# Optimization experiments

Hardware: AMD Instinct MI355X
Metric: run time of the kernel (lower is better)

## Reference

```python
import jax, jax.numpy as jnp
import numpy as np

B_, S_, IN_, D_, N_, K_ = 16, 4096, 64, 256, 16, 32


def _ln(x, g, b):
    m = jnp.mean(x, axis=-1, keepdims=True)
    v = jnp.var(x, axis=-1, keepdims=True)
    return (x - m) * jax.lax.rsqrt(v + 1e-5) * g + b


def setup_inputs() -> dict:
    key = jax.random.key(0)
    ks = jax.random.split(key, 24)
    s = 0.02
    d = dict(
        x=jax.random.normal(ks[0], (B_, S_, IN_), jnp.float32),
        W_in=jax.random.normal(ks[1], (IN_, D_)) * s, b_in=jnp.zeros((D_,)),
        ln1_g=jnp.ones((D_,)), ln1_b=jnp.zeros((D_,)),
        conv_w=jax.random.normal(ks[2], (D_, 1, 3)) * s, conv_b=jnp.zeros((D_,)),
        Wd=jax.random.normal(ks[3], (D_, D_)) * s, bd=jnp.zeros((D_,)),
        WB=jax.random.normal(ks[4], (D_, N_)) * s, bB=jnp.zeros((N_,)),
        WC=jax.random.normal(ks[5], (D_, N_)) * s, bC=jnp.zeros((N_,)),
        A=-jax.random.uniform(ks[6], (D_, N_)),
        Wg=jax.random.normal(ks[7], (D_, D_)) * s, bg=jnp.zeros((D_,)),
        filt_re=jax.random.normal(ks[8], (K_, D_)) * s,
        filt_im=jax.random.normal(ks[9], (K_, D_)) * s,
        alpha=jnp.ones((D_,)), beta=jnp.ones((D_,)),
        lnc_g=jnp.ones((D_,)), lnc_b=jnp.zeros((D_,)),
        W1=jax.random.normal(ks[10], (D_, D_ // 2)) * s, b1=jnp.zeros((D_ // 2,)),
        W2=jax.random.normal(ks[11], (D_ // 2, 2)) * s, b2=jnp.zeros((2,)),
    )
    return d


def reference(x, W_in, b_in, ln1_g, ln1_b, conv_w, conv_b, Wd, bd, WB, bB, WC, bC,
              A, Wg, bg, filt_re, filt_im, alpha, beta, lnc_g, lnc_b, W1, b1, W2, b2):
    xp = x @ W_in + b_in                                   # [B,S,D]

    # ---- TemporalBlock ----
    xn = _ln(xp, ln1_g, ln1_b)
    xc = jax.lax.conv_general_dilated(
        jnp.swapaxes(xn, 1, 2), conv_w, (1,), [(1, 1)],
        feature_group_count=D_, dimension_numbers=('NCH', 'OIH', 'NCH'))
    xc = jnp.swapaxes(xc + conv_b[:, None], 1, 2)          # [B,S,D]
    u = jax.nn.silu(xc)

    delta = jax.nn.softplus(u @ Wd + bd)                   # [B,S,D]
    Bm = u @ WB + bB                                       # [B,S,N]
    Cm = u @ WC + bC                                       # [B,S,N]

    def step(h, inp):
        u_t, d_t, B_t, C_t = inp                           # [B,D],[B,D],[B,N],[B,N]
        h = (1.0 + d_t[:, :, None] * A) * h + d_t[:, :, None] * B_t[:, None, :] * u_t[:, :, None]
        y_t = jnp.sum(C_t[:, None, :] * h, axis=-1)        # [B,D]
        return h, y_t

    h0 = jnp.zeros((u.shape[0], D_, N_), u.dtype)
    xs = tuple(jnp.swapaxes(a, 0, 1) for a in (u, delta, Bm, Cm))
    _, ys = jax.lax.scan(step, h0, xs)
    x_ssm = jnp.swapaxes(ys, 0, 1)                         # [B,S,D]
    g = jax.nn.silu(xn @ Wg + bg)
    x_t = xp + x_ssm * g

    # ---- SpectralBlock ----
    Xf = jnp.fft.rfft(xp, axis=1)                          # [B,F,D] complex
    mag = jnp.abs(Xf)
    _, idx = jax.lax.top_k(jnp.swapaxes(mag, 1, 2), K_)    # [B,D,K]
    idx = jnp.swapaxes(idx, 1, 2)                          # [B,K,D]
    sel = jnp.take_along_axis(Xf, idx, axis=1)             # [B,K,D]
    filt = filt_re + 1j * filt_im                          # [K,D]
    filtered = sel * filt[None]
    bi = jnp.arange(Xf.shape[0])[:, None, None]
    di = jnp.arange(D_)[None, None, :]
    Xfil = jnp.zeros_like(Xf).at[bi, idx, di].set(filtered)
    x_f = jnp.fft.irfft(Xfil, n=xp.shape[1], axis=1)       # [B,S,D]

    # ---- Fusion + classifier (eval: dropout = identity) ----
    z = alpha * x_t + beta * x_f
    zp = jnp.mean(z, axis=1)                               # [B,D]
    hcls = jax.nn.relu(_ln(zp, lnc_g, lnc_b) @ W1 + b1)
    return hcls @ W2 + b2                                  # [B,2]
```

## Files before the change

kernel.cpp:

```cpp
#include <hip/hip_runtime.h>
#include <hip/hip_bf16.h>
#include <math.h>

#define BB 16
#define SS 4096
#define IN 64
#define DD 256
#define NN 16
#define KK 32
#define CH 64
#define LCH 64
#define BS (BB*SS)

typedef __attribute__((ext_vector_type(4))) float f32x4;
typedef __attribute__((ext_vector_type(8))) short bf16x8;

__device__ __forceinline__ float bf2f(unsigned short u){
  return __uint_as_float(((unsigned int)u)<<16);
}
__device__ __forceinline__ unsigned short f2bf(float f){
  unsigned int u = __float_as_uint(f);
  return (unsigned short)((u + 0x7fffu + ((u>>16)&1u)) >> 16);
}
__device__ __forceinline__ float fast_softplus(float v){
  float e = __expf(-fabsf(v));
  return fmaxf(v, 0.f) + __logf(1.f + e);
}
__device__ __forceinline__ float fast_silu(float v){
  return v * __builtin_amdgcn_rcpf(1.f + __expf(-v));
}
__device__ __forceinline__ void* swz(void* base, int row, int byteoff){
  return (void*)((char*)base + (row<<9) + (byteoff ^ ((row&7)<<4)));
}
#define SW(i) ((i) ^ (((i)>>4)&15))
__device__ __forceinline__ int rev4(int k){
  return ((k&3)<<10) | (((k>>2)&3)<<8) | (((k>>4)&3)<<6)
       | (((k>>6)&3)<<4) | (((k>>8)&3)<<2) | ((k>>10)&3);
}

__global__ void k_prep(const float* Wd, const float* Wg, const float* WB, const float* WC,
                       const float* W_in, const float* bBv, const float* bCv,
                       unsigned short* WdF, unsigned short* WgF, unsigned short* WinF,
                       float* bbc, float2* tw){
  int id = blockIdx.x*256 + threadIdx.x;
  if (id < 73728){
    int jn = id >> 12; int rem = id & 4095;
    int kc = rem >> 9; int l8 = (rem >> 3) & 63; int e = id & 7;
    int lr = l8 & 15, lh = l8 >> 4;
    int k = kc*32 + lh*8 + e;
    float v;
    if (jn < 16){ int n = jn*16 + lr; v = Wd[k*256+n]; }
    else { int c = (jn-16)*16 + lr; v = (c<16) ? WB[k*16+c] : WC[k*16+(c-16)]; }
    WdF[id] = f2bf(v);
  }
  else if (id < 139264){
    int o = id - 73728;
    int jn = o >> 12; int rem = o & 4095;
    int kc = rem >> 9; int l8 = (rem >> 3) & 63; int e = o & 7;
    int lr = l8 & 15, lh = l8 >> 4;
    int k = kc*32 + lh*8 + e;
    WgF[o] = f2bf(Wg[k*256 + jn*16 + lr]);
  }
  else if (id < 155648){
    int o = id - 139264;
    int jn = o >> 10; int rem = o & 1023;
    int kc = rem >> 9; int l8 = (rem >> 3) & 63; int e = o & 7;
    int lr = l8 & 15, lh = l8 >> 4;
    int k = kc*32 + lh*8 + e;
    WinF[o] = f2bf(W_in[k*256 + jn*16 + lr]);
  }
  else if (id < 157696){ int k = id-155648;
    double a = -6.283185307179586476925287 * (double)k / 4096.0;
    tw[k] = make_float2((float)cos(a), (float)sin(a)); }
  else if (id < 157728){ int j = id-157696; bbc[j] = (j<16)? bBv[j] : bCv[j-16]; }
}

__global__ __launch_bounds__(256) void k_front(const float* x, const unsigned short* WinF, const float* b_in,
      const float* ln1_g, const float* ln1_b, const float* conv_w, const float* conv_b,
      float2* xpz, unsigned short* xn16, unsigned short* u16){
  __shared__ unsigned short xb[32*64];
  __shared__ float xs[20][260];
  int tid = threadIdx.x;
  int b = blockIdx.y; int t0 = blockIdx.x*16;
  {
    int row = tid>>3, slot = tid&7;
    int t = t0 - 1 + row;
    unsigned short h[8];
    if (row < 18 && t >= 0 && t < SS){
      const float* src = &x[((size_t)b*SS + t)*IN + slot*8];
      float4 v0 = *(const float4*)src;
      float4 v1 = *(const float4*)(src+4);
      h[0]=f2bf(v0.x); h[1]=f2bf(v0.y); h[2]=f2bf(v0.z); h[3]=f2bf(v0.w);
      h[4]=f2bf(v1.x); h[5]=f2bf(v1.y); h[6]=f2bf(v1.z); h[7]=f2bf(v1.w);
    } else {
      #pragma unroll
      for (int i=0;i<8;i++) h[i]=0;
    }
    *(uint4*)&xb[row*64 + ((slot ^ (row&7))<<3)] = *(uint4*)h;
  }
  __syncthreads();
  int wv = tid>>6, lane = tid&63, lr = lane&15, lh = lane>>4;
  {
    bf16x8 af[2][2];
    #pragma unroll
    for (int rf=0;rf<2;rf++)
      #pragma unroll
      for (int kc=0;kc<2;kc++){
        int row = rf*16 + lr;
        int slot = (kc*4 + lh) ^ (row&7);
        af[rf][kc] = *(const bf16x8*)&xb[row*64 + slot*8];
      }
    f32x4 acc[2][4];
    #pragma unroll
    for (int rf=0;rf<2;rf++)
      #pragma unroll
      for (int jj=0;jj<4;jj++){ acc[rf][jj][0]=0.f; acc[rf][jj][1]=0.f; acc[rf][jj][2]=0.f; acc[rf][jj][3]=0.f; }
    #pragma unroll
    for (int jj=0;jj<4;jj++){
      int jn = wv*4 + jj;
      const bf16x8* bp = (const bf16x8*)(WinF + (size_t)jn*1024 + (size_t)lane*8);
      bf16x8 b0 = bp[0];
      bf16x8 b1 = bp[64];
      #pragma unroll
      for (int rf=0;rf<2;rf++){
        acc[rf][jj] = __builtin_amdgcn_mfma_f32_16x16x32_bf16(af[rf][0], b0, acc[rf][jj], 0,0,0);
        acc[rf][jj] = __builtin_amdgcn_mfma_f32_16x16x32_bf16(af[rf][1], b1, acc[rf][jj], 0,0,0);
      }
    }
    #pragma unroll
    for (int jj=0;jj<4;jj++){
      int col = (wv*4+jj)*16 + lr;
      float bs = b_in[col];
      #pragma unroll
      for (int rf=0;rf<2;rf++){
        #pragma unroll
        for (int i=0;i<4;i++){
          int row = rf*16 + lh*4 + i;
          if (row < 18) xs[row][col] = acc[rf][jj][i] + bs;
        }
      }
    }
  }
  __syncthreads();
  {
    int sl = tid&15, p0 = tid>>4;
    float2* dst = xpz + (size_t)b*128*SS + t0 + sl;
    #pragma unroll
    for (int pass=0; pass<8; pass++){
      int p = p0 + 16*pass;
      float2 v = *(const float2*)&xs[1+sl][2*p];
      dst[(size_t)p*SS] = v;
    }
  }
  __syncthreads();
  float4 lg4 = *(const float4*)&ln1_g[lane*4];
  float4 lb4 = *(const float4*)&ln1_b[lane*4];
  for (int r=wv; r<18; r+=4){
    int t = t0 - 1 + r;
    bool valid = (t>=0) && (t<SS);
    float4 v = *(const float4*)&xs[r][lane*4];
    float s1 = v.x+v.y+v.z+v.w;
    float s2 = v.x*v.x+v.y*v.y+v.z*v.z+v.w*v.w;
    #pragma unroll
    for (int off=32; off; off>>=1){ s1 += __shfl_xor(s1,off); s2 += __shfl_xor(s2,off); }
    float mean = s1*(1.f/256.f);
    float var  = s2*(1.f/256.f) - mean*mean;
    float rstd = rsqrtf(var + 1e-5f);
    float o0 = valid ? ((v.x-mean)*rstd*lg4.x + lb4.x) : 0.f;
    float o1 = valid ? ((v.y-mean)*rstd*lg4.y + lb4.y) : 0.f;
    float o2 = valid ? ((v.z-mean)*rstd*lg4.z + lb4.z) : 0.f;
    float o3 = valid ? ((v.w-mean)*rstd*lg4.w + lb4.w) : 0.f;
    *(float4*)&xs[r][lane*4] = make_float4(o0,o1,o2,o3);
    if (r>=1 && r<=16){
      ushort4 st;
      st.x=f2bf(o0); st.y=f2bf(o1); st.z=f2bf(o2); st.w=f2bf(o3);
      *(ushort4*)&xn16[((size_t)b*SS + t)*DD + lane*4] = st;
    }
  }
  __syncthreads();
  int d = tid;
  float w0=conv_w[d*3], w1=conv_w[d*3+1], w2=conv_w[d*3+2], cb=conv_b[d];
  #pragma unroll 4
  for (int rr=0; rr<16; rr++){
    float a0=xs[rr][d], a1=xs[rr+1][d], a2=xs[rr+2][d];
    float xc = a0*w0 + a1*w1 + a2*w2 + cb;
    u16[((size_t)b*SS + (t0+rr))*DD + d] = f2bf(fast_silu(xc));
  }
}

template<int NTOT, int ACT>
__global__ __launch_bounds__(512,2) void k_gemm2(const unsigned short* Ab, const unsigned short* Bt,
      const float* bias_main, const float* bias_bc,
      unsigned short* out_main, unsigned short* out_bc){
  __shared__ unsigned short As[64*256];
  const int NF = NTOT/2;
  int tid = threadIdx.x;
  int m0 = blockIdx.x*64;
  {
    const uint4* gA = (const uint4*)(Ab + (size_t)m0*256);
    #pragma unroll
    for (int i=0;i<4;i++){
      int f = tid + 512*i;
      uint4 v = gA[f];
      *(uint4*)swz(As, f>>5, (f&31)<<4) = v;
    }
  }
  __syncthreads();
  int wv = tid>>6, lane = tid&63;
  int wm = wv>>1, nh = wv&1;
  int lr = lane&15, lh = lane>>4;
  const bf16x8* bbase = (const bf16x8*)(Bt + (size_t)(nh*NF)*4096 + (size_t)lane*8);
  f32x4 acc[NF];
  #pragma unroll
  for (int j=0;j<NF;j++){ acc[j][0]=0.f; acc[j][1]=0.f; acc[j][2]=0.f; acc[j][3]=0.f; }
  bf16x8 bq[2][8];
  #pragma unroll
  for (int kc=0;kc<8;kc++) bq[0][kc] = bbase[kc*64];
  #pragma unroll
  for (int j=0;j<NF;j++){
    if (j+1 < NF){
      #pragma unroll
      for (int kc=0;kc<8;kc++) bq[(j+1)&1][kc] = bbase[(j+1)*512 + kc*64];
    }
    #pragma unroll
    for (int kc=0;kc<8;kc++){
      bf16x8 af = *(const bf16x8*)swz(As, wm*16+lr, kc*64+lh*16);
      acc[j] = __builtin_amdgcn_mfma_f32_16x16x32_bf16(af, bq[j&1][kc], acc[j], 0,0,0);
    }
  }
  #pragma unroll
  for (int j=0;j<NF;j++){
    int jn = nh*NF + j;
    if (jn < 16){
      int col = jn*16 + lr;
      float bs = bias_main[col];
      #pragma unroll
      for (int i=0;i<4;i++){
        int row = m0 + wm*16 + lh*4 + i;
        float v = acc[j][i] + bs;
        if (ACT==1) v = fast_softplus(v);
        if (ACT==2) v = fast_silu(v);
        out_main[(size_t)row*256 + col] = f2bf(v);
      }
    } else {
      int col = (jn-16)*16 + lr;
      float bs = bias_bc[col];
      #pragma unroll
      for (int i=0;i<4;i++){
        int row = m0 + wm*16 + lh*4 + i;
        out_bc[(size_t)row*32 + col] = f2bf(acc[j][i] + bs);
      }
    }
  }
}

__global__ __launch_bounds__(256,4) void k_fft(const float2* xpz, const float2* twg, int* rank, float* T0){
  __shared__ float2 buf[4096];
  __shared__ int scr8[8];
  int blk = blockIdx.x;
  int b = blk >> 7, pair = blk & 127;
  int tid = threadIdx.x;
  const float4* src4 = (const float4*)(xpz + ((size_t)b*128 + pair)*SS);
  #pragma unroll
  for (int q=tid; q<2048; q+=256){
    float4 v = src4[q];
    buf[SW(2*q)]   = make_float2(v.x, v.y);
    buf[SW(2*q+1)] = make_float2(v.z, v.w);
  }
  __syncthreads();
  int m = 1024, fac = 1;
  for (int st=0; st<6; st++){
    #pragma unroll
    for (int it=0; it<4; it++){
      int t = tid + 256*it;
      int j = t & (m-1);
      int i0 = 4*t - 3*j;
      float2 a0 = buf[SW(i0)];
      float2 a1 = buf[SW(i0+m)];
      float2 a2 = buf[SW(i0+2*m)];
      float2 a3 = buf[SW(i0+3*m)];
      float2 w1 = twg[j*fac];
      float2 w2 = make_float2(fmaf(w1.x,w1.x,-w1.y*w1.y), 2.f*w1.x*w1.y);
      float2 w3 = make_float2(fmaf(w1.x,w2.x,-w1.y*w2.y), fmaf(w1.x,w2.y, w1.y*w2.x));
      float t0x=a0.x+a2.x, t0y=a0.y+a2.y;
      float t1x=a0.x-a2.x, t1y=a0.y-a2.y;
      float t2x=a1.x+a3.x, t2y=a1.y+a3.y;
      float t3x=a1.y-a3.y, t3y=a3.x-a1.x;
      buf[SW(i0)]     = make_float2(t0x+t2x, t0y+t2y);
      float b1x = t1x+t3x, b1y = t1y+t3y;
      buf[SW(i0+m)]   = make_float2(fmaf(w1.x,b1x,-w1.y*b1y), fmaf(w1.x,b1y, w1.y*b1x));
      float b2x = t0x-t2x, b2y = t0y-t2y;
      buf[SW(i0+2*m)] = make_float2(fmaf(w2.x,b2x,-w2.y*b2y), fmaf(w2.x,b2y, w2.y*b2x));
      float b3x = t1x-t3x, b3y = t1y-t3y;
      buf[SW(i0+3*m)] = make_float2(fmaf(w3.x,b3x,-w3.y*b3y), fmaf(w3.x,b3y, w3.y*b3x));
    }
    __syncthreads();
    m >>= 2; fac <<= 2;
  }
  float2 z0 = buf[0];
  float thx = 4.f*z0.x*z0.x, thy = 4.f*z0.y*z0.y;
  int cx=0, cy=0;
  #pragma unroll
  for (int j=0;j<8;j++){
    int f = 1 + tid + 256*j;
    float2 zf = buf[SW(rev4(f))];
    float2 zc = buf[SW(rev4(4096-f))];
    float sxr = zf.x+zc.x, sxi = zf.y-zc.y;
    float syr = zf.x-zc.x, syi = zf.y+zc.y;
    cx += (fmaf(sxr,sxr,sxi*sxi) > thx) ? 1 : 0;
    cy += (fmaf(syr,syr,syi*syi) > thy) ? 1 : 0;
  }
  #pragma unroll
  for (int off=32; off; off>>=1){ cx += __shfl_xor(cx, off); cy += __shfl_xor(cy, off); }
  if ((tid&63)==0){ scr8[tid>>6] = cx; scr8[4+(tid>>6)] = cy; }
  __syncthreads();
  if (tid==0){
    int r0 = b*256 + 2*pair;
    rank[r0]   = scr8[0]+scr8[1]+scr8[2]+scr8[3];
    rank[r0+1] = scr8[4]+scr8[5]+scr8[6]+scr8[7];
    T0[r0]   = z0.x;
    T0[r0+1] = z0.y;
  }
}

__global__ __launch_bounds__(512) void k_scanA(const unsigned short* d16, const unsigned short* u16,
      const unsigned short* bc16, const float* Aw, float* AB_A, float* AB_B){
  __shared__ float bcs[LCH][16];
  int c = blockIdx.x, b = blockIdx.y;
  int t0 = c*LCH;
  int tid = threadIdx.x;
  {
    int t = tid>>3, q = tid&7;
    unsigned int v = *(const unsigned int*)(bc16 + ((size_t)b*SS + t0 + t)*32 + q*2);
    bcs[t][q*2]   = bf2f((unsigned short)(v & 0xffff));
    bcs[t][q*2+1] = bf2f((unsigned short)(v >> 16));
  }
  __syncthreads();
  int d = tid & 255, hf = tid >> 8;
  float aw[8];
  #pragma unroll
  for (int j=0;j<2;j++){
    float4 a4 = *(const float4*)&Aw[d*16 + hf*8 + j*4];
    aw[4*j]=a4.x; aw[4*j+1]=a4.y; aw[4*j+2]=a4.z; aw[4*j+3]=a4.w;
  }
  float Ac[8], Bc[8];
  #pragma unroll
  for (int n=0;n<8;n++){ Ac[n]=1.f; Bc[n]=0.f; }
  const unsigned short* dp = d16 + ((size_t)b*SS + t0)*DD + d;
  const unsigned short* up = u16 + ((size_t)b*SS + t0)*DD + d;
  #pragma unroll 8
  for (int t=0;t<LCH;t++){
    float de = bf2f(dp[(size_t)t*DD]);
    float uu = bf2f(up[(size_t)t*DD]);
    float du = de*uu;
    float4 b0 = *(const float4*)&bcs[t][hf*8];
    float4 b1 = *(const float4*)&bcs[t][hf*8+4];
    float bm[8] = {b0.x,b0.y,b0.z,b0.w, b1.x,b1.y,b1.z,b1.w};
    #pragma unroll
    for (int n=0;n<8;n++){
      float a = fmaf(de, aw[n], 1.f);
      Ac[n] *= a;
      Bc[n] = fmaf(a, Bc[n], du*bm[n]);
    }
  }
  size_t o = (size_t)c*65536 + (size_t)b*4096 + (size_t)d*16 + hf*8;
  #pragma unroll
  for (int j=0;j<2;j++){
    *(float4*)&AB_A[o+4*j] = make_float4(Ac[4*j],Ac[4*j+1],Ac[4*j+2],Ac[4*j+3]);
    *(float4*)&AB_B[o+4*j] = make_float4(Bc[4*j],Bc[4*j+1],Bc[4*j+2],Bc[4*j+3]);
  }
}

__global__ void k_scanB(const float* AB_A, const float* AB_B, float* Hs){
  int tid = blockIdx.x*256 + threadIdx.x;
  float h = 0.f;
  #pragma unroll 8
  for (int c=0;c<CH;c++){
    Hs[c*65536 + tid] = h;
    h = fmaf(AB_A[c*65536 + tid], h, AB_B[c*65536 + tid]);
  }
}

__global__ __launch_bounds__(512) void k_scanC(const unsigned short* d16, const unsigned short* u16,
      const unsigned short* bc16, const unsigned short* g16, const float* Aw, const float* Hs, float* part){
  __shared__ float bcs[LCH][32];
  __shared__ float scr[256];
  int c = blockIdx.x, b = blockIdx.y;
  int t0 = c*LCH;
  int tid = threadIdx.x;
  {
    int t = tid>>3, q = tid&7;
    uint2 v = *(const uint2*)(bc16 + ((size_t)b*SS + t0 + t)*32 + q*4);
    bcs[t][q*4]   = bf2f((unsigned short)(v.x & 0xffff));
    bcs[t][q*4+1] = bf2f((unsigned short)(v.x >> 16));
    bcs[t][q*4+2] = bf2f((unsigned short)(v.y & 0xffff));
    bcs[t][q*4+3] = bf2f((unsigned short)(v.y >> 16));
  }
  __syncthreads();
  int d = tid & 255, hf = tid >> 8;
  float aw[8];
  #pragma unroll
  for (int j=0;j<2;j++){
    float4 a4 = *(const float4*)&Aw[d*16 + hf*8 + j*4];
    aw[4*j]=a4.x; aw[4*j+1]=a4.y; aw[4*j+2]=a4.z; aw[4*j+3]=a4.w;
  }
  float h[8];
  {
    size_t o = (size_t)c*65536 + (size_t)b*4096 + (size_t)d*16 + hf*8;
    #pragma unroll
    for (int j=0;j<2;j++){
      float4 h4 = *(const float4*)&Hs[o+4*j];
      h[4*j]=h4.x; h[4*j+1]=h4.y; h[4*j+2]=h4.z; h[4*j+3]=h4.w;
    }
  }
  float acc = 0.f;
  const unsigned short* dp = d16 + ((size_t)b*SS + t0)*DD + d;
  const unsigned short* up = u16 + ((size_t)b*SS + t0)*DD + d;
  const unsigned short* gp = g16 + ((size_t)b*SS + t0)*DD + d;
  #pragma unroll 8
  for (int t=0;t<LCH;t++){
    float de = bf2f(dp[(size_t)t*DD]);
    float uu = bf2f(up[(size_t)t*DD]);
    float gg = bf2f(gp[(size_t)t*DD]);
    float du = de*uu;
    float4 b0 = *(const float4*)&bcs[t][hf*8];
    float4 b1 = *(const float4*)&bcs[t][hf*8+4];
    float4 c0 = *(const float4*)&bcs[t][16+hf*8];
    float4 c1 = *(const float4*)&bcs[t][16+hf*8+4];
    float bm[8] = {b0.x,b0.y,b0.z,b0.w, b1.x,b1.y,b1.z,b1.w};
    float cm[8] = {c0.x,c0.y,c0.z,c0.w, c1.x,c1.y,c1.z,c1.w};
    float y0 = 0.f, y1 = 0.f;
    #pragma unroll
    for (int n=0;n<8;n+=2){
      float a0 = fmaf(de, aw[n],   1.f);
      float a1 = fmaf(de, aw[n+1], 1.f);
      h[n]   = fmaf(a0, h[n],   du*bm[n]);
      h[n+1] = fmaf(a1, h[n+1], du*bm[n+1]);
      y0 = fmaf(cm[n],   h[n],   y0);
      y1 = fmaf(cm[n+1], h[n+1], y1);
    }
    acc = fmaf(y0+y1, gg, acc);
  }
  if (hf==1) scr[d] = acc;
  __syncthreads();
  if (hf==0) part[(size_t)(b*256 + d)*CH + c] = acc + scr[d];
}

__global__ __launch_bounds__(256) void k_final(const float* part, const float* T0, const int* rank,
      const float* alpha, const float* beta, const float* filt_re,
      const float* lnc_g, const float* lnc_b,
      const float* W1, const float* b1, const float* W2, const float* b2,
      float* out){
  __shared__ float zs[256];
  __shared__ float h1[128];
  __shared__ float red[8];
  int b = blockIdx.x, d = threadIdx.x;
  int row = b*256 + d;
  float ps = 0.f;
  #pragma unroll 8
  for (int c=0;c<CH;c++) ps += part[(size_t)row*CH + c];
  float ssm_mean = ps * (1.f/4096.f);
  float t0v = T0[row];
  float mxp = t0v * (1.f/4096.f);
  int r = rank[row];
  float spec = (r < KK) ? t0v * filt_re[r*DD + d] * (1.f/4096.f) : 0.f;
  float zp = alpha[d]*(mxp + ssm_mean) + beta[d]*spec;
  float s1 = zp, s2 = zp*zp;
  #pragma unroll
  for (int off=32; off; off>>=1){ s1 += __shfl_xor(s1,off); s2 += __shfl_xor(s2,off); }
  if ((d&63)==0){ red[d>>6] = s1; red[4+(d>>6)] = s2; }
  __syncthreads();
  float mean = (red[0]+red[1]+red[2]+red[3]) * (1.f/256.f);
  float var  = (red[4]+red[5]+red[6]+red[7]) * (1.f/256.f) - mean*mean;
  float ln = (zp-mean)*rsqrtf(var+1e-5f)*lnc_g[d] + lnc_b[d];
  zs[d] = ln;
  __syncthreads();
  if (d < 128){
    float acc = b1[d];
    #pragma unroll 16
    for (int k=0;k<256;k++) acc = fmaf(zs[k], W1[k*128+d], acc);
    h1[d] = fmaxf(acc, 0.f);
  }
  __syncthreads();
  if (d < 2){
    float acc = b2[d];
    #pragma unroll 16
    for (int k=0;k<128;k++) acc = fmaf(h1[k], W2[k*2+d], acc);
    out[b*2+d] = acc;
  }
}

extern "C" void kernel_launch(void* const* d_in, const int* in_sizes, int n_in,
                              void* d_out, int out_size, void* d_ws, size_t ws_size,
                              hipStream_t stream){
  const float* x      = (const float*)d_in[0];
  const float* W_in   = (const float*)d_in[1];
  const float* b_in   = (const float*)d_in[2];
  const float* ln1_g  = (const float*)d_in[3];
  const float* ln1_b  = (const float*)d_in[4];
  const float* conv_w = (const float*)d_in[5];
  const float* conv_b = (const float*)d_in[6];
  const float* Wd     = (const float*)d_in[7];
  const float* bd     = (const float*)d_in[8];
  const float* WB     = (const float*)d_in[9];
  const float* bB     = (const float*)d_in[10];
  const float* WC     = (const float*)d_in[11];
  const float* bC     = (const float*)d_in[12];
  const float* A      = (const float*)d_in[13];
  const float* Wg     = (const float*)d_in[14];
  const float* bg     = (const float*)d_in[15];
  const float* filt_re= (const float*)d_in[16];
  const float* alpha  = (const float*)d_in[18];
  const float* beta   = (const float*)d_in[19];
  const float* lnc_g  = (const float*)d_in[20];
  const float* lnc_b  = (const float*)d_in[21];
  const float* W1     = (const float*)d_in[22];
  const float* b1     = (const float*)d_in[23];
  const float* W2     = (const float*)d_in[24];
  const float* b2     = (const float*)d_in[25];

  char* w = (char*)d_ws;
  unsigned short* d16  = (unsigned short*)(w);
  unsigned short* bc16 = (unsigned short*)(w + 33554432);
  float2* xpz = (float2*)(w + 67108864);
  float* AB_A = (float*)(w + 67108864);
  float* AB_B = (float*)(w + 67108864 + 16777216);
  float* Hs   = (float*)(w + 67108864 + 33554432);
  float* part = (float*)(w + 67108864 + 50331648);
  unsigned short* xn16 = (unsigned short*)(w + 134217728);
  unsigned short* u16  = (unsigned short*)(w + 167772160);
  unsigned short* g16  = (unsigned short*)(w + 201326592);
  char* small = w + 234881024;
  unsigned short* WdF  = (unsigned short*)(small);
  unsigned short* WgF  = (unsigned short*)(small + 147456);
  unsigned short* WinF = (unsigned short*)(small + 278528);
  float*  bbc = (float*)(small + 311296);
  float2* tw  = (float2*)(small + 311424);
  float*  T0  = (float*)(small + 327808);
  int*    rank= (int*)(small + 344192);
  (void)in_sizes; (void)n_in; (void)out_size; (void)ws_size;

  hipLaunchKernelGGL(k_prep, dim3(617), dim3(256), 0, stream,
                     Wd, Wg, WB, WC, W_in, bB, bC, WdF, WgF, WinF, bbc, tw);
  hipLaunchKernelGGL(k_front, dim3(SS/16, BB), dim3(256), 0, stream,
                     x, WinF, b_in, ln1_g, ln1_b, conv_w, conv_b, xpz, xn16, u16);
  hipLaunchKernelGGL(k_fft, dim3(BB*128), dim3(256), 0, stream, xpz, tw, rank, T0);
  hipLaunchKernelGGL((k_gemm2<18,1>), dim3(BS/64), dim3(512), 0, stream,
                     u16, WdF, bd, bbc, d16, bc16);
  hipLaunchKernelGGL((k_gemm2<16,2>), dim3(BS/64), dim3(512), 0, stream,
                     xn16, WgF, bg, bbc, g16, bc16);
  hipLaunchKernelGGL(k_scanA, dim3(CH, BB), dim3(512), 0, stream, d16, u16, bc16, A, AB_A, AB_B);
  hipLaunchKernelGGL(k_scanB, dim3(256), dim3(256), 0, stream, AB_A, AB_B, Hs);
  hipLaunchKernelGGL(k_scanC, dim3(CH, BB), dim3(512), 0, stream, d16, u16, bc16, g16, A, Hs, part);
  hipLaunchKernelGGL(k_final, dim3(BB), dim3(256), 0, stream,
                     part, T0, rank, alpha, beta, filt_re, lnc_g, lnc_b, W1, b1, W2, b2, (float*)d_out);
}
```

Measured before the change: 251.8 us.

## Store delta, delta*u and gate transposed time-major for vectorized scan loads

The GEMM epilogues now write delta, delta*u (using u already staged in shared memory) and the silu gate in a [B,D,S] transposed layout with 4-wide stores. The scan kernels then read 8 consecutive timesteps per 16-byte load per channel, instead of strided scalar bf16 loads across D, and no longer reload u. The bc16 buffer is moved to make room. In exchange the GEMM stores are strided across channels and less coalesced, and du is rounded to bf16 after the multiply.

```diff
diff --git a/kernel.cpp b/kernel.cpp
--- a/kernel.cpp
+++ b/kernel.cpp
@@ -191,7 +191,7 @@
 template<int NTOT, int ACT>
 __global__ __launch_bounds__(512,2) void k_gemm2(const unsigned short* Ab, const unsigned short* Bt,
       const float* bias_main, const float* bias_bc,
-      unsigned short* out_main, unsigned short* out_bc){
+      unsigned short* outT, unsigned short* duT, unsigned short* out_bc){
   __shared__ unsigned short As[64*256];
   const int NF = NTOT/2;
   int tid = threadIdx.x;
@@ -228,19 +228,33 @@
       acc[j] = __builtin_amdgcn_mfma_f32_16x16x32_bf16(af, bq[j&1][kc], acc[j], 0,0,0);
     }
   }
+  int row0 = m0 + wm*16 + lh*4;
+  int bb = row0 >> 12, tb = row0 & 4095;
   #pragma unroll
   for (int j=0;j<NF;j++){
     int jn = nh*NF + j;
     if (jn < 16){
       int col = jn*16 + lr;
       float bs = bias_main[col];
-      #pragma unroll
-      for (int i=0;i<4;i++){
-        int row = m0 + wm*16 + lh*4 + i;
-        float v = acc[j][i] + bs;
-        if (ACT==1) v = fast_softplus(v);
-        if (ACT==2) v = fast_silu(v);
-        out_main[(size_t)row*256 + col] = f2bf(v);
+      if (ACT==1){
+        ushort4 de4, du4;
+        unsigned short* dep = (unsigned short*)&de4;
+        unsigned short* dup = (unsigned short*)&du4;
+        #pragma unroll
+        for (int i=0;i<4;i++){
+          float de = fast_softplus(acc[j][i] + bs);
+          float uu = bf2f(*(const unsigned short*)swz(As, wm*16+lh*4+i, col*2));
+          dep[i] = f2bf(de);
+          dup[i] = f2bf(de*uu);
+        }
+        *(ushort4*)&outT[((size_t)bb*256 + col)*SS + tb] = de4;
+        *(ushort4*)&duT [((size_t)bb*256 + col)*SS + tb] = du4;
+      } else {
+        ushort4 g4;
+        unsigned short* gp = (unsigned short*)&g4;
+        #pragma unroll
+        for (int i=0;i<4;i++) gp[i] = f2bf(fast_silu(acc[j][i] + bs));
+        *(ushort4*)&outT[((size_t)bb*256 + col)*SS + tb] = g4;
       }
     } else {
       int col = (jn-16)*16 + lr;
@@ -323,7 +337,7 @@
   }
 }
 
-__global__ __launch_bounds__(512) void k_scanA(const unsigned short* d16, const unsigned short* u16,
+__global__ __launch_bounds__(512) void k_scanA(const unsigned short* deT, const unsigned short* duT,
       const unsigned short* bc16, const float* Aw, float* AB_A, float* AB_B){
   __shared__ float bcs[LCH][16];
   int c = blockIdx.x, b = blockIdx.y;
@@ -346,21 +360,41 @@
   float Ac[8], Bc[8];
   #pragma unroll
   for (int n=0;n<8;n++){ Ac[n]=1.f; Bc[n]=0.f; }
-  const unsigned short* dp = d16 + ((size_t)b*SS + t0)*DD + d;
-  const unsigned short* up = u16 + ((size_t)b*SS + t0)*DD + d;
-  #pragma unroll 8
-  for (int t=0;t<LCH;t++){
-    float de = bf2f(dp[(size_t)t*DD]);
-    float uu = bf2f(up[(size_t)t*DD]);
-    float du = de*uu;
-    float4 b0 = *(const float4*)&bcs[t][hf*8];
-    float4 b1 = *(const float4*)&bcs[t][hf*8+4];
-    float bm[8] = {b0.x,b0.y,b0.z,b0.w, b1.x,b1.y,b1.z,b1.w};
-    #pragma unroll
-    for (int n=0;n<8;n++){
-      float a = fmaf(de, aw[n], 1.f);
-      Ac[n] *= a;
-      Bc[n] = fmaf(a, Bc[n], du*bm[n]);
+  const uint4* dp4 = (const uint4*)(deT + ((size_t)(b*256+d))*SS + t0);
+  const uint4* up4 = (const uint4*)(duT + ((size_t)(b*256+d))*SS + t0);
+  uint4 dv[2], uv[2];
+  dv[0] = dp4[0]; uv[0] = up4[0];
+  #pragma unroll
+  for (int q8=0; q8<8; q8++){
+    int cur = q8&1;
+    if (q8 < 7){ dv[cur^1] = dp4[q8+1]; uv[cur^1] = up4[q8+1]; }
+    const unsigned int* dw = (const unsigned int*)&dv[cur];
+    const unsigned int* uw = (const unsigned int*)&uv[cur];
+    #pragma unroll
+    for (int e=0;e<4;e++){
+      int t = q8*8 + e*2;
+      float de0 = __uint_as_float(dw[e]<<16);
+      float de1 = __uint_as_float(dw[e]&0xffff0000u);
+      float du0 = __uint_as_float(uw[e]<<16);
+      float du1 = __uint_as_float(uw[e]&0xffff0000u);
+      float4 b0 = *(const float4*)&bcs[t][hf*8];
+      float4 b1 = *(const float4*)&bcs[t][hf*8+4];
+      float4 b2 = *(const float4*)&bcs[t+1][hf*8];
+      float4 b3 = *(const float4*)&bcs[t+1][hf*8+4];
+      float bm0[8] = {b0.x,b0.y,b0.z,b0.w, b1.x,b1.y,b1.z,b1.w};
+      float bm1[8] = {b2.x,b2.y,b2.z,b2.w, b3.x,b3.y,b3.z,b3.w};
+      #pragma unroll
+      for (int n=0;n<8;n++){
+        float a = fmaf(de0, aw[n], 1.f);
+        Ac[n] *= a;
+        Bc[n] = fmaf(a, Bc[n], du0*bm0[n]);
+      }
+      #pragma unroll
+      for (int n=0;n<8;n++){
+        float a = fmaf(de1, aw[n], 1.f);
+        Ac[n] *= a;
+        Bc[n] = fmaf(a, Bc[n], du1*bm1[n]);
+      }
     }
   }
   size_t o = (size_t)c*65536 + (size_t)b*4096 + (size_t)d*16 + hf*8;
@@ -381,8 +415,8 @@
   }
 }
 
-__global__ __launch_bounds__(512) void k_scanC(const unsigned short* d16, const unsigned short* u16,
-      const unsigned short* bc16, const unsigned short* g16, const float* Aw, const float* Hs, float* part){
+__global__ __launch_bounds__(512) void k_scanC(const unsigned short* deT, const unsigned short* duT,
+      const unsigned short* bc16, const unsigned short* gT, const float* Aw, const float* Hs, float* part){
   __shared__ float bcs[LCH][32];
   __shared__ float scr[256];
   int c = blockIdx.x, b = blockIdx.y;
@@ -414,32 +448,66 @@
     }
   }
   float acc = 0.f;
-  const unsigned short* dp = d16 + ((size_t)b*SS + t0)*DD + d;
-  const unsigned short* up = u16 + ((size_t)b*SS + t0)*DD + d;
-  const unsigned short* gp = g16 + ((size_t)b*SS + t0)*DD + d;
-  #pragma unroll 8
-  for (int t=0;t<LCH;t++){
-    float de = bf2f(dp[(size_t)t*DD]);
-    float uu = bf2f(up[(size_t)t*DD]);
-    float gg = bf2f(gp[(size_t)t*DD]);
-    float du = de*uu;
-    float4 b0 = *(const float4*)&bcs[t][hf*8];
-    float4 b1 = *(const float4*)&bcs[t][hf*8+4];
-    float4 c0 = *(const float4*)&bcs[t][16+hf*8];
-    float4 c1 = *(const float4*)&bcs[t][16+hf*8+4];
-    float bm[8] = {b0.x,b0.y,b0.z,b0.w, b1.x,b1.y,b1.z,b1.w};
-    float cm[8] = {c0.x,c0.y,c0.z,c0.w, c1.x,c1.y,c1.z,c1.w};
-    float y0 = 0.f, y1 = 0.f;
-    #pragma unroll
-    for (int n=0;n<8;n+=2){
-      float a0 = fmaf(de, aw[n],   1.f);
-      float a1 = fmaf(de, aw[n+1], 1.f);
-      h[n]   = fmaf(a0, h[n],   du*bm[n]);
-      h[n+1] = fmaf(a1, h[n+1], du*bm[n+1]);
-      y0 = fmaf(cm[n],   h[n],   y0);
-      y1 = fmaf(cm[n+1], h[n+1], y1);
-    }
-    acc = fmaf(y0+y1, gg, acc);
+  const uint4* dp4 = (const uint4*)(deT + ((size_t)(b*256+d))*SS + t0);
+  const uint4* up4 = (const uint4*)(duT + ((size_t)(b*256+d))*SS + t0);
+  const uint4* gp4 = (const uint4*)(gT  + ((size_t)(b*256+d))*SS + t0);
+  uint4 dv[2], uv[2], gv[2];
+  dv[0] = dp4[0]; uv[0] = up4[0]; gv[0] = gp4[0];
+  #pragma unroll
+  for (int q8=0; q8<8; q8++){
+    int cur = q8&1;
+    if (q8 < 7){ dv[cur^1] = dp4[q8+1]; uv[cur^1] = up4[q8+1]; gv[cur^1] = gp4[q8+1]; }
+    const unsigned int* dw = (const unsigned int*)&dv[cur];
+    const unsigned int* uw = (const unsigned int*)&uv[cur];
+    const unsigned int* gw = (const unsigned int*)&gv[cur];
+    #pragma unroll
+    for (int e=0;e<4;e++){
+      int t = q8*8 + e*2;
+      float de0 = __uint_as_float(dw[e]<<16);
+      float de1 = __uint_as_float(dw[e]&0xffff0000u);
+      float du0 = __uint_as_float(uw[e]<<16);
+      float du1 = __uint_as_float(uw[e]&0xffff0000u);
+      float gg0 = __uint_as_float(gw[e]<<16);
+      float gg1 = __uint_as_float(gw[e]&0xffff0000u);
+      {
+        float4 b0 = *(const float4*)&bcs[t][hf*8];
+        float4 b1 = *(const float4*)&bcs[t][hf*8+4];
+        float4 c0 = *(const float4*)&bcs[t][16+hf*8];
+        float4 c1 = *(const float4*)&bcs[t][16+hf*8+4];
+        float bm[8] = {b0.x,b0.y,b0.z,b0.w, b1.x,b1.y,b1.z,b1.w};
+        float cm[8] = {c0.x,c0.y,c0.z,c0.w, c1.x,c1.y,c1.z,c1.w};
+        float y0 = 0.f, y1 = 0.f;
+        #pragma unroll
+        for (int n=0;n<8;n+=2){
+          float a0 = fmaf(de0, aw[n],   1.f);
+          float a1 = fmaf(de0, aw[n+1], 1.f);
+          h[n]   = fmaf(a0, h[n],   du0*bm[n]);
+          h[n+1] = fmaf(a1, h[n+1], du0*bm[n+1]);
+          y0 = fmaf(cm[n],   h[n],   y0);
+          y1 = fmaf(cm[n+1], h[n+1], y1);
+        }
+        acc = fmaf(y0+y1, gg0, acc);
+      }
+      {
+        float4 b0 = *(const float4*)&bcs[t+1][hf*8];
+        float4 b1 = *(const float4*)&bcs[t+1][hf*8+4];
+        float4 c0 = *(const float4*)&bcs[t+1][16+hf*8];
+        float4 c1 = *(const float4*)&bcs[t+1][16+hf*8+4];
+        float bm[8] = {b0.x,b0.y,b0.z,b0.w, b1.x,b1.y,b1.z,b1.w};
+        float cm[8] = {c0.x,c0.y,c0.z,c0.w, c1.x,c1.y,c1.z,c1.w};
+        float y0 = 0.f, y1 = 0.f;
+        #pragma unroll
+        for (int n=0;n<8;n+=2){
+          float a0 = fmaf(de1, aw[n],   1.f);
+          float a1 = fmaf(de1, aw[n+1], 1.f);
+          h[n]   = fmaf(a0, h[n],   du1*bm[n]);
+          h[n+1] = fmaf(a1, h[n+1], du1*bm[n+1]);
+          y0 = fmaf(cm[n],   h[n],   y0);
+          y1 = fmaf(cm[n+1], h[n+1], y1);
+        }
+        acc = fmaf(y0+y1, gg1, acc);
+      }
+    }
   }
   if (hf==1) scr[d] = acc;
   __syncthreads();
@@ -520,16 +588,17 @@
   const float* b2     = (const float*)d_in[25];
 
   char* w = (char*)d_ws;
-  unsigned short* d16  = (unsigned short*)(w);
-  unsigned short* bc16 = (unsigned short*)(w + 33554432);
+  unsigned short* deT  = (unsigned short*)(w);
+  unsigned short* duT  = (unsigned short*)(w + 33554432);
   float2* xpz = (float2*)(w + 67108864);
   float* AB_A = (float*)(w + 67108864);
   float* AB_B = (float*)(w + 67108864 + 16777216);
   float* Hs   = (float*)(w + 67108864 + 33554432);
-  float* part = (float*)(w + 67108864 + 50331648);
+  unsigned short* bc16 = (unsigned short*)(w + 67108864 + 50331648);
+  float* part = (float*)(w + 67108864 + 54525952);
   unsigned short* xn16 = (unsigned short*)(w + 134217728);
   unsigned short* u16  = (unsigned short*)(w + 167772160);
-  unsigned short* g16  = (unsigned short*)(w + 201326592);
+  unsigned short* gT   = (unsigned short*)(w + 201326592);
   char* small = w + 234881024;
   unsigned short* WdF  = (unsigned short*)(small);
   unsigned short* WgF  = (unsigned short*)(small + 147456);
@@ -546,12 +615,12 @@
                      x, WinF, b_in, ln1_g, ln1_b, conv_w, conv_b, xpz, xn16, u16);
   hipLaunchKernelGGL(k_fft, dim3(BB*128), dim3(256), 0, stream, xpz, tw, rank, T0);
   hipLaunchKernelGGL((k_gemm2<18,1>), dim3(BS/64), dim3(512), 0, stream,
-                     u16, WdF, bd, bbc, d16, bc16);
+                     u16, WdF, bd, bbc, deT, duT, bc16);
   hipLaunchKernelGGL((k_gemm2<16,2>), dim3(BS/64), dim3(512), 0, stream,
-                     xn16, WgF, bg, bbc, g16, bc16);
-  hipLaunchKernelGGL(k_scanA, dim3(CH, BB), dim3(512), 0, stream, d16, u16, bc16, A, AB_A, AB_B);
+                     xn16, WgF, bg, bbc, gT, (unsigned short*)nullptr, bc16);
+  hipLaunchKernelGGL(k_scanA, dim3(CH, BB), dim3(512), 0, stream, deT, duT, bc16, A, AB_A, AB_B);
   hipLaunchKernelGGL(k_scanB, dim3(256), dim3(256), 0, stream, AB_A, AB_B, Hs);
-  hipLaunchKernelGGL(k_scanC, dim3(CH, BB), dim3(512), 0, stream, d16, u16, bc16, g16, A, Hs, part);
+  hipLaunchKernelGGL(k_scanC, dim3(CH, BB), dim3(512), 0, stream, deT, duT, bc16, gT, A, Hs, part);
   hipLaunchKernelGGL(k_final, dim3(BB), dim3(256), 0, stream,
                      part, T0, rank, alpha, beta, filt_re, lnc_g, lnc_b, W1, b1, W2, b2, (float*)d_out);
 }
```

Measured after the change: 342.3 us. +35.9%, slower.
